# Kernel optimization log

Hardware: AMD Instinct MI355X
Metric: run time of the kernel (lower is better)

Reference implementation:

```python
import jax, jax.numpy as jnp
import numpy as np

B, M, A, NS, T = 256, 16, 4096, 1024, 64
DT = 0.001          # dt
DA = DT             # da == dt
REF_T = 0.004       # refractory period (s)
SYN_DELAY_BINS = 1  # floor(syn_delay / da)
N_NEUR = 500.0      # neurons per population (self.N)
A_GRID = jnp.linspace(0.0, A * DA, A + 1)[:-1]  # (A,) ages since last spike


def _get_plam(input_total, V_old, age, rp, amem, ft):
    # V_old: (B,M,K); input_total: (B,M,1); age broadcasts against (B,M,K)
    V_new = V_old + DA * (rp - V_old) * amem + DA * input_total
    V_new = jnp.where(age < REF_T, 0.0, V_new)
    lam = jnp.where(V_new == 0.0, 1e-8, jnp.exp(V_new - ft))  # firing intensity
    p = lam * DT
    Plam = jnp.where(p >= 0.01, 1.0 - jnp.exp(-p), p)
    return V_new, Plam, lam


def setup_inputs() -> dict:
    key = jax.random.key(0)
    ks = jax.random.split(key, 13)
    return {
        "x": jax.random.normal(ks[0], (B, M), jnp.float32),
        "V_t_old": jax.random.normal(ks[1], (B, M, A), jnp.float32),
        "logS_t_old": jax.random.normal(ks[2], (B, M, A), jnp.float32),
        "sampled_neuron_v": jax.random.normal(ks[3], (B, M, NS), jnp.float32),
        "sampled_neuron_lastfire": jax.random.uniform(ks[4], (B, M, NS), jnp.float32),
        "I_syn": jax.random.uniform(ks[5], (B, M, 1), jnp.float32),
        "amem": jax.random.uniform(ks[6], (M, 1), jnp.float32),
        "asyn": jax.random.uniform(ks[7], (M, 1), jnp.float32),
        "J": jax.random.normal(ks[8], (M, M), jnp.float32),
        "rp": jax.random.uniform(ks[9], (M, 1), jnp.float32),
        "ft": jax.random.uniform(ks[10], (M, 1), jnp.float32),
        "eps": jax.random.uniform(ks[11], (1,), jnp.float32),
        "Z_hist_est": jnp.clip(jax.random.uniform(ks[12], (B, M, A + T), jnp.float32), 1e-5, 1.0),
        "internal_clock": 32,
    }


def reference(x, V_t_old, logS_t_old, sampled_neuron_v, sampled_neuron_lastfire,
              I_syn, amem, asyn, J, rp, ft, eps, Z_hist_est, internal_clock):
    clk = int(internal_clock)
    # ---- synaptic current with exponential decay and delayed pop activity ----
    exp_syn = jnp.exp(-DT * asyn)  # (M,1)
    if clk > SYN_DELAY_BINS:
        Z_t_last = Z_hist_est[:, :, clk + A - SYN_DELAY_BINS - 1:clk + A - SYN_DELAY_BINS]
        I_syn = exp_syn * I_syn + (1.0 - exp_syn) * Z_t_last / DT
    # input_total: (B,M,1)
    input_total = jnp.einsum('bm,mn->bn', I_syn[:, :, 0], J)[:, :, None] + (x * eps)[:, :, None]

    # ---- population activity update ----
    Z_t = Z_hist_est[:, :, clk:clk + A][:, :, ::-1]          # (B,M,A), youngest age first
    Z_t_new = Z_hist_est[:, :, clk + A:clk + A + 1]          # (B,M,1)

    V_t_new, Plam, _ = _get_plam(input_total, V_t_old, A_GRID, rp, amem, ft)

    S_old = jnp.exp(logS_t_old)
    m_t = S_old * Z_t
    Zmacro = jnp.sum(m_t * Plam, axis=2, keepdims=True)
    mess = 1.0 - jnp.sum(m_t, axis=2, keepdims=True)
    v_t = (1.0 - S_old) * m_t
    num = jnp.sum(v_t * Plam, axis=2, keepdims=True)
    den = jnp.sum(v_t, axis=2, keepdims=True)
    lambda_t = jnp.where(den != 0.0, num / jnp.where(den == 0.0, 1.0, den), 0.0)  # nan -> 0
    Z = jnp.clip(Zmacro + lambda_t * mess, 0.0, 1.0)
    A_t = Z / DT
    var = Z / N_NEUR + 0.1 * DT / N_NEUR
    Z_nll = 0.5 * jnp.square(Z_t_new - Z) / var + 0.5 * jnp.log(var) + 0.5 * jnp.log(2.0 * 3.14)

    # ---- sampled-neuron spike likelihood ----
    snv_new, Plam_s, lam_s = _get_plam(input_total, sampled_neuron_v, sampled_neuron_lastfire, rp, amem, ft)
    ltdt = lam_s * DT
    lnPy = jnp.where(ltdt < 0.01, snv_new - ft + jnp.log(DT), jnp.log(Plam_s))
    lnP1_y = -ltdt

    return (A_t, Z, Z_nll, lnPy, lnP1_y, V_t_new, snv_new, I_syn)
```

## Files before the change

### kernel.cpp

```cpp
#include <hip/hip_runtime.h>

#define B_   256
#define M_   16
#define A_   4096
#define NS_  1024
#define T_   64
#define AT_  (A_ + T_)

static constexpr float DTc = 0.001f;
static constexpr float DAc = 0.001f;

static constexpr size_t OFF_AT    = 0;
static constexpr size_t OFF_Z     = 4096;
static constexpr size_t OFF_ZNLL  = 8192;
static constexpr size_t OFF_LNPY  = 12288;
static constexpr size_t OFF_LNP1Y = 12288 + 4194304;
static constexpr size_t OFF_VT    = 12288 + 2ull * 4194304;
static constexpr size_t OFF_SNV   = OFF_VT + 16777216ull;
static constexpr size_t OFF_ISYN  = OFF_SNV + 4194304ull;

__global__ __launch_bounds__(256) void lif_kernel(
    const float* __restrict__ x,
    const float* __restrict__ V_t_old,
    const float* __restrict__ logS_t_old,
    const float* __restrict__ snv_in,
    const float* __restrict__ snlf,
    const float* __restrict__ I_syn,
    const float* __restrict__ amem,
    const float* __restrict__ asyn,
    const float* __restrict__ J,
    const float* __restrict__ rp,
    const float* __restrict__ ft,
    const float* __restrict__ eps,
    const float* __restrict__ Z_hist,
    const int*   __restrict__ clk_ptr,
    float* __restrict__ out)
{
    const int row = blockIdx.x;
    const int b   = row >> 4;
    const int m   = row & 15;
    const int tid = threadIdx.x;

    __shared__ float sh_I[M_];
    __shared__ float sh_inT;
    __shared__ float sh_red[4][4];

    const int clk = *clk_ptr;

    if (tid < M_) {
        float es   = expf(-DTc * asyn[tid]);
        float Iold = I_syn[b * M_ + tid];
        float In   = Iold;
        if (clk > 1) {
            float zl = Z_hist[(size_t)(b * M_ + tid) * AT_ + (clk + A_ - 2)];
            In = es * Iold + (1.0f - es) * zl / DTc;
        }
        sh_I[tid] = In;
    }
    __syncthreads();
    if (tid == 0) {
        float dot = 0.0f;
#pragma unroll
        for (int mm = 0; mm < M_; ++mm) dot += sh_I[mm] * J[mm * M_ + m];
        sh_inT = dot + x[row] * eps[0];
        out[OFF_ISYN + row] = sh_I[m];
    }
    __syncthreads();

    const float a_m  = amem[m];
    const float rp_m = rp[m];
    const float ft_m = ft[m];
    const float inT  = sh_inT;

    const size_t rowA = (size_t)row * A_;
    const size_t rowZ = (size_t)row * AT_;

    float sZm = 0.0f, sM = 0.0f, sNum = 0.0f, sDen = 0.0f;

#pragma unroll
    for (int c = 0; c < 4; ++c) {
        const int a0 = c * 1024 + tid * 4;
        const float4 vo = *reinterpret_cast<const float4*>(V_t_old    + rowA + a0);
        const float4 ls = *reinterpret_cast<const float4*>(logS_t_old + rowA + a0);
        const float vov[4] = {vo.x, vo.y, vo.z, vo.w};
        const float lsv[4] = {ls.x, ls.y, ls.z, ls.w};
        const float* zp = Z_hist + rowZ + (clk + A_ - 1 - a0);
        float vres[4];
#pragma unroll
        for (int k = 0; k < 4; ++k) {
            const int a = a0 + k;
            float V = vov[k] + DAc * (rp_m - vov[k]) * a_m + DAc * inT;
            if (a < 4) V = 0.0f;
            float lam  = (V == 0.0f) ? 1e-8f : expf(V - ft_m);
            float p    = lam * DTc;
            float Plam = (p >= 0.01f) ? (1.0f - expf(-p)) : p;
            float S    = expf(lsv[k]);
            float z    = zp[-k];
            float mt   = S * z;
            sZm += mt * Plam;
            sM  += mt;
            float v = (1.0f - S) * mt;
            sNum += v * Plam;
            sDen += v;
            vres[k] = V;
        }
        *reinterpret_cast<float4*>(out + OFF_VT + rowA + a0) =
            make_float4(vres[0], vres[1], vres[2], vres[3]);
    }

    float vals[4] = {sZm, sM, sNum, sDen};
#pragma unroll
    for (int i = 0; i < 4; ++i) {
        float v = vals[i];
        for (int off = 32; off > 0; off >>= 1) v += __shfl_down(v, off, 64);
        vals[i] = v;
    }
    const int wave = tid >> 6, lane = tid & 63;
    if (lane == 0) {
#pragma unroll
        for (int i = 0; i < 4; ++i) sh_red[wave][i] = vals[i];
    }
    __syncthreads();
    if (tid == 0) {
        float Zm  = sh_red[0][0] + sh_red[1][0] + sh_red[2][0] + sh_red[3][0];
        float sMt = sh_red[0][1] + sh_red[1][1] + sh_red[2][1] + sh_red[3][1];
        float num = sh_red[0][2] + sh_red[1][2] + sh_red[2][2] + sh_red[3][2];
        float den = sh_red[0][3] + sh_red[1][3] + sh_red[2][3] + sh_red[3][3];
        float mess  = 1.0f - sMt;
        float lam_t = (den != 0.0f) ? (num / den) : 0.0f;
        float Z = Zm + lam_t * mess;
        Z = fminf(fmaxf(Z, 0.0f), 1.0f);
        float At  = Z / DTc;
        float var = Z / 500.0f + 0.1f * DTc / 500.0f;
        float ztn = Z_hist[rowZ + clk + A_];
        float d   = ztn - Z;
        float znll = 0.5f * (d * d) / var + 0.5f * logf(var) + 0.5f * logf(2.0f * 3.14f);
        out[OFF_AT   + row] = At;
        out[OFF_Z    + row] = Z;
        out[OFF_ZNLL + row] = znll;
    }

    {
        const size_t rowS = (size_t)row * NS_;
        const int s0 = tid * 4;
        const float4 v4  = *reinterpret_cast<const float4*>(snv_in + rowS + s0);
        const float4 lf4 = *reinterpret_cast<const float4*>(snlf   + rowS + s0);
        const float vv[4] = {v4.x, v4.y, v4.z, v4.w};
        const float lf[4] = {lf4.x, lf4.y, lf4.z, lf4.w};
        float vn[4], py[4], p1[4];
#pragma unroll
        for (int k = 0; k < 4; ++k) {
            float V = vv[k] + DAc * (rp_m - vv[k]) * a_m + DAc * inT;
            if (lf[k] < 0.004f) V = 0.0f;
            float lam  = (V == 0.0f) ? 1e-8f : expf(V - ft_m);
            float ltdt = lam * DTc;
            float Plam = (ltdt >= 0.01f) ? (1.0f - expf(-ltdt)) : ltdt;
            py[k] = (ltdt < 0.01f) ? (V - ft_m + logf(DTc)) : logf(Plam);
            p1[k] = -ltdt;
            vn[k] = V;
        }
        *reinterpret_cast<float4*>(out + OFF_SNV   + rowS + s0) = make_float4(vn[0], vn[1], vn[2], vn[3]);
        *reinterpret_cast<float4*>(out + OFF_LNPY  + rowS + s0) = make_float4(py[0], py[1], py[2], py[3]);
        *reinterpret_cast<float4*>(out + OFF_LNP1Y + rowS + s0) = make_float4(p1[0], p1[1], p1[2], p1[3]);
    }
}

extern "C" void kernel_launch(void* const* d_in, const int* in_sizes, int n_in,
                              void* d_out, int out_size, void* d_ws, size_t ws_size,
                              hipStream_t stream) {
    lif_kernel<<<B_ * M_, 256, 0, stream>>>(
        (const float*)d_in[0],
        (const float*)d_in[1],
        (const float*)d_in[2],
        (const float*)d_in[3],
        (const float*)d_in[4],
        (const float*)d_in[5],
        (const float*)d_in[6],
        (const float*)d_in[7],
        (const float*)d_in[8],
        (const float*)d_in[9],
        (const float*)d_in[10],
        (const float*)d_in[11],
        (const float*)d_in[12],
        (const int*)  d_in[13],
        (float*)d_out);
}
```

Before: 312.0 us.

## Prefetch next chunk, vectorize Z loads, use nontemporal stores and shuffle dot

Software-pipelines the per-row streaming loop by loading the next 1024-element chunk of V, logS and the Z history while the current chunk is computed. Z history reads become one float4 load reversed in registers when the clock is 4-aligned. Output writes use nontemporal stores, the sampled-neuron loads are issued before the reduction barrier, the 16-term J dot product moves to a lane shuffle, and the launch bounds request 8 blocks per CU. The extra prefetch registers could hurt occupancy, and nontemporal stores only help if they actually avoid cache pollution.

After: 320.9 us. 1.03x slower.

```diff
diff --git a/kernel.cpp b/kernel.cpp
--- a/kernel.cpp
+++ b/kernel.cpp
@@ -9,6 +9,7 @@
 
 static constexpr float DTc = 0.001f;
 static constexpr float DAc = 0.001f;
+static constexpr float LOG_DT = -6.907755278982137f;
 
 static constexpr size_t OFF_AT    = 0;
 static constexpr size_t OFF_Z     = 4096;
@@ -19,7 +20,14 @@
 static constexpr size_t OFF_SNV   = OFF_VT + 16777216ull;
 static constexpr size_t OFF_ISYN  = OFF_SNV + 4194304ull;
 
-__global__ __launch_bounds__(256) void lif_kernel(
+typedef float v4f __attribute__((ext_vector_type(4)));
+
+static __device__ __forceinline__ void nt_store4(float* p, float a, float b, float c, float d) {
+    v4f v; v.x = a; v.y = b; v.z = c; v.w = d;
+    __builtin_nontemporal_store(v, reinterpret_cast<v4f*>(p));
+}
+
+__global__ __launch_bounds__(256, 8) void lif_kernel(
     const float* __restrict__ x,
     const float* __restrict__ V_t_old,
     const float* __restrict__ logS_t_old,
@@ -58,12 +66,14 @@
         sh_I[tid] = In;
     }
     __syncthreads();
-    if (tid == 0) {
-        float dot = 0.0f;
-#pragma unroll
-        for (int mm = 0; mm < M_; ++mm) dot += sh_I[mm] * J[mm * M_ + m];
-        sh_inT = dot + x[row] * eps[0];
-        out[OFF_ISYN + row] = sh_I[m];
+    if (tid < M_) {
+        float t = sh_I[tid] * J[tid * M_ + m];
+#pragma unroll
+        for (int off = 8; off > 0; off >>= 1) t += __shfl_down(t, off, 16);
+        if (tid == 0) {
+            sh_inT = t + x[row] * eps[0];
+            out[OFF_ISYN + row] = sh_I[m];
+        }
     }
     __syncthreads();
 
@@ -75,16 +85,36 @@
     const size_t rowA = (size_t)row * A_;
     const size_t rowZ = (size_t)row * AT_;
 
-    float sZm = 0.0f, sM = 0.0f, sNum = 0.0f, sDen = 0.0f;
+    const bool zal = ((clk & 3) == 0);
+
+    const float* pV = V_t_old    + rowA + tid * 4;
+    const float* pS = logS_t_old + rowA + tid * 4;
+    const float* pZ = Z_hist     + rowZ + (clk + A_ - 4 - tid * 4);
+
+    float4 vc = *reinterpret_cast<const float4*>(pV);
+    float4 sc = *reinterpret_cast<const float4*>(pS);
+    float4 zc = zal ? *reinterpret_cast<const float4*>(pZ)
+                    : make_float4(pZ[0], pZ[1], pZ[2], pZ[3]);
+
+    float sZm = 0.0f, sMt = 0.0f, sNum = 0.0f, sDen = 0.0f;
 
 #pragma unroll
     for (int c = 0; c < 4; ++c) {
+        float4 vn_, sn_, zn_;
+        if (c < 3) {
+            const float* qV = pV + (c + 1) * 1024;
+            const float* qS = pS + (c + 1) * 1024;
+            const float* qZ = pZ - (c + 1) * 1024;
+            vn_ = *reinterpret_cast<const float4*>(qV);
+            sn_ = *reinterpret_cast<const float4*>(qS);
+            zn_ = zal ? *reinterpret_cast<const float4*>(qZ)
+                      : make_float4(qZ[0], qZ[1], qZ[2], qZ[3]);
+        }
+
         const int a0 = c * 1024 + tid * 4;
-        const float4 vo = *reinterpret_cast<const float4*>(V_t_old    + rowA + a0);
-        const float4 ls = *reinterpret_cast<const float4*>(logS_t_old + rowA + a0);
-        const float vov[4] = {vo.x, vo.y, vo.z, vo.w};
-        const float lsv[4] = {ls.x, ls.y, ls.z, ls.w};
-        const float* zp = Z_hist + rowZ + (clk + A_ - 1 - a0);
+        const float vov[4]  = {vc.x, vc.y, vc.z, vc.w};
+        const float lsv[4]  = {sc.x, sc.y, sc.z, sc.w};
+        const float zrev[4] = {zc.w, zc.z, zc.y, zc.x};
         float vres[4];
 #pragma unroll
         for (int k = 0; k < 4; ++k) {
@@ -95,20 +125,24 @@
             float p    = lam * DTc;
             float Plam = (p >= 0.01f) ? (1.0f - expf(-p)) : p;
             float S    = expf(lsv[k]);
-            float z    = zp[-k];
-            float mt   = S * z;
+            float mt   = S * zrev[k];
             sZm += mt * Plam;
-            sM  += mt;
+            sMt += mt;
             float v = (1.0f - S) * mt;
             sNum += v * Plam;
             sDen += v;
             vres[k] = V;
         }
-        *reinterpret_cast<float4*>(out + OFF_VT + rowA + a0) =
-            make_float4(vres[0], vres[1], vres[2], vres[3]);
-    }
-
-    float vals[4] = {sZm, sM, sNum, sDen};
+        nt_store4(out + OFF_VT + rowA + a0, vres[0], vres[1], vres[2], vres[3]);
+        vc = vn_; sc = sn_; zc = zn_;
+    }
+
+    const size_t rowS = (size_t)row * NS_;
+    const int s0 = tid * 4;
+    const float4 v4  = *reinterpret_cast<const float4*>(snv_in + rowS + s0);
+    const float4 lf4 = *reinterpret_cast<const float4*>(snlf   + rowS + s0);
+
+    float vals[4] = {sZm, sMt, sNum, sDen};
 #pragma unroll
     for (int i = 0; i < 4; ++i) {
         float v = vals[i];
@@ -123,10 +157,10 @@
     __syncthreads();
     if (tid == 0) {
         float Zm  = sh_red[0][0] + sh_red[1][0] + sh_red[2][0] + sh_red[3][0];
-        float sMt = sh_red[0][1] + sh_red[1][1] + sh_red[2][1] + sh_red[3][1];
+        float sM  = sh_red[0][1] + sh_red[1][1] + sh_red[2][1] + sh_red[3][1];
         float num = sh_red[0][2] + sh_red[1][2] + sh_red[2][2] + sh_red[3][2];
         float den = sh_red[0][3] + sh_red[1][3] + sh_red[2][3] + sh_red[3][3];
-        float mess  = 1.0f - sMt;
+        float mess  = 1.0f - sM;
         float lam_t = (den != 0.0f) ? (num / den) : 0.0f;
         float Z = Zm + lam_t * mess;
         Z = fminf(fmaxf(Z, 0.0f), 1.0f);
@@ -141,10 +175,6 @@
     }
 
     {
-        const size_t rowS = (size_t)row * NS_;
-        const int s0 = tid * 4;
-        const float4 v4  = *reinterpret_cast<const float4*>(snv_in + rowS + s0);
-        const float4 lf4 = *reinterpret_cast<const float4*>(snlf   + rowS + s0);
         const float vv[4] = {v4.x, v4.y, v4.z, v4.w};
         const float lf[4] = {lf4.x, lf4.y, lf4.z, lf4.w};
         float vn[4], py[4], p1[4];
@@ -155,13 +185,13 @@
             float lam  = (V == 0.0f) ? 1e-8f : expf(V - ft_m);
             float ltdt = lam * DTc;
             float Plam = (ltdt >= 0.01f) ? (1.0f - expf(-ltdt)) : ltdt;
-            py[k] = (ltdt < 0.01f) ? (V - ft_m + logf(DTc)) : logf(Plam);
+            py[k] = (ltdt < 0.01f) ? (V - ft_m + LOG_DT) : logf(Plam);
             p1[k] = -ltdt;
             vn[k] = V;
         }
-        *reinterpret_cast<float4*>(out + OFF_SNV   + rowS + s0) = make_float4(vn[0], vn[1], vn[2], vn[3]);
-        *reinterpret_cast<float4*>(out + OFF_LNPY  + rowS + s0) = make_float4(py[0], py[1], py[2], py[3]);
-        *reinterpret_cast<float4*>(out + OFF_LNP1Y + rowS + s0) = make_float4(p1[0], p1[1], p1[2], p1[3]);
+        nt_store4(out + OFF_SNV   + rowS + s0, vn[0], vn[1], vn[2], vn[3]);
+        nt_store4(out + OFF_LNPY  + rowS + s0, py[0], py[1], py[2], py[3]);
+        nt_store4(out + OFF_LNP1Y + rowS + s0, p1[0], p1[1], p1[2], p1[3]);
     }
 }
 
```
